# Optimization experiments

Measured on AMD Instinct MI355X. Metric: run time of the kernel, lower is better.

## Reference

```python
import jax, jax.numpy as jnp
import numpy as np

N, DEG, F_IN, H = 50000, 16, 128, 32
E = N * DEG


def _linear_params(key, out_f, in_f):
    kw, kb = jax.random.split(key)
    s = 1.0 / np.sqrt(in_f)
    W = jax.random.uniform(kw, (out_f, in_f), jnp.float32, -s, s)
    b = jax.random.uniform(kb, (out_f,), jnp.float32, -s, s)
    return W, b


def setup_inputs() -> dict:
    key = jax.random.key(0)
    ks = jax.random.split(key, 12)
    X = jax.random.normal(ks[0], (N, F_IN), jnp.float32)
    # DEG distinct nonzero offsets shared by all rows -> unique (src,dst) pairs,
    # so the COO tensor is already coalesced (no duplicate indices).
    offsets = jax.random.permutation(ks[1], jnp.arange(1, N))[:DEG]
    src = jnp.repeat(jnp.arange(N, dtype=jnp.int32), DEG)
    dst = ((src.reshape(N, DEG) + offsets[None, :].astype(jnp.int32)) % N).reshape(-1)
    D = jax.ops.segment_sum(jnp.ones((E,), jnp.float32), src, num_segments=N)
    wn1p, bn1p = _linear_params(ks[2], H, F_IN)      # convN1.pass_map
    wn1s, bn1s = _linear_params(ks[3], H, F_IN)      # convN1.self_map
    we1p, be1p = _linear_params(ks[4], H, 2 * H)     # convE1.pass_map
    we1s, be1s = _linear_params(ks[5], H, F_IN)      # convE1.self_map
    wn2p, bn2p = _linear_params(ks[6], H, H)         # convN2.pass_map
    wn2s, bn2s = _linear_params(ks[7], H, H)         # convN2.self_map
    we2p, be2p = _linear_params(ks[8], H, 2 * H)     # convE2.pass_map
    we2s, be2s = _linear_params(ks[9], H, H)         # convE2.self_map
    wc, bc = _linear_params(ks[10], 1, H)            # classifier
    return dict(X=X, src=src, dst=dst, D=D,
                wn1p=wn1p, bn1p=bn1p, wn1s=wn1s, bn1s=bn1s,
                we1p=we1p, be1p=be1p, we1s=we1s, be1s=be1s,
                wn2p=wn2p, bn2p=bn2p, wn2s=wn2s, bn2s=bn2s,
                we2p=we2p, be2p=be2p, we2s=we2s, be2s=be2s,
                wc=wc, bc=bc)


def reference(X, src, dst, D,
              wn1p, bn1p, wn1s, bn1s,
              we1p, be1p, we1s, be1s,
              wn2p, bn2p, wn2s, bn2s,
              we2p, be2p, we2s, be2s,
              wc, bc):
    n = X.shape[0]

    def node_conv(vals, Xn, wp, bp, ws, bs):
        # torch.sparse.sum(A, dim=1): sum edge values per source row
        Asum = jax.ops.segment_sum(vals, src, num_segments=n)
        return jax.nn.relu((Asum / D[:, None]) @ wp.T + bp + Xn @ ws.T + bs)

    def edge_conv(vals, Xn, wp, bp, ws, bs):
        X1, X2 = Xn[src], Xn[dst]
        Ef = jnp.concatenate([(X1 - X2) * 0.5, (X1 + X2) * 0.5], axis=-1)
        return jax.nn.relu(Ef @ wp.T + bp + vals @ ws.T + bs)

    # add_graph: edge features = |X[src] - X[dst]|
    vals0 = jnp.abs(X[src] - X[dst])            # (E, F_IN)
    X0 = jnp.zeros_like(X)                       # forward zeros node features
    Xn1 = node_conv(vals0, X0, wn1p, bn1p, wn1s, bn1s)   # (N, 32)
    vals1 = edge_conv(vals0, Xn1, we1p, be1p, we1s, be1s)  # (E, 32)
    Xn2 = node_conv(vals1, Xn1, wn2p, bn2p, wn2s, bn2s)  # (N, 32)
    vals2 = edge_conv(vals1, Xn2, we2p, be2p, we2s, be2s)  # (E, 32)
    SX = jax.nn.sigmoid(vals2 @ wc.T + bc)[:, 0]          # (E,)
    return SX
```

## Files before the change

### kernel.cpp

```cpp
#include <hip/hip_runtime.h>

#define DEG 16
#define F_IN 128
#define H 32

typedef __attribute__((ext_vector_type(8))) _Float16 f16x8;
typedef __attribute__((ext_vector_type(4))) float f32x4;
typedef __attribute__((ext_vector_type(4))) int i32x4;

union HS  { _Float16 f; unsigned short s; };
union HF4 { _Float16 h[4]; uint2 u; };

__device__ __forceinline__ float relu_f(float x) { return fmaxf(x, 0.0f); }

__device__ __forceinline__ f16x8 habs8(f16x8 a) {
    union { f16x8 h; i32x4 i; } u; u.h = a;
#pragma unroll
    for (int k = 0; k < 4; ++k) u.i[k] &= 0x7FFF7FFF;
    return u.h;
}

__global__ __launch_bounds__(256) void k_pre(
    const float* __restrict__ X, _Float16* __restrict__ Xh, long n8,
    const float* __restrict__ we1s, const float* __restrict__ we1p,
    const float* __restrict__ be1p, const float* __restrict__ be1s,
    const float* __restrict__ we2p, const float* __restrict__ we2s,
    const float* __restrict__ be2p, const float* __restrict__ be2s,
    const float* __restrict__ wn1p, const float* __restrict__ bn1p,
    const float* __restrict__ bn1s,
    const float* __restrict__ wn2p, const float* __restrict__ bn2p,
    const float* __restrict__ wn2s, const float* __restrict__ bn2s,
    _Float16* __restrict__ Wcat1, _Float16* __restrict__ Wcat2,
    _Float16* __restrict__ Wn1ph,
    _Float16* __restrict__ Wn2ph, _Float16* __restrict__ Wn2sh,
    float* __restrict__ bias1, float* __restrict__ bias2,
    float* __restrict__ biasn1, float* __restrict__ biasn2)
{
    if (blockIdx.x >= 32) {
        const long t = (long)(blockIdx.x - 32) * 256 + threadIdx.x;
        if (t >= n8) return;
        const float4* p = (const float4*)X + t * 2;
        const float4 a = p[0], b = p[1];
        f16x8 h;
        h[0] = (_Float16)a.x; h[1] = (_Float16)a.y; h[2] = (_Float16)a.z; h[3] = (_Float16)a.w;
        h[4] = (_Float16)b.x; h[5] = (_Float16)b.y; h[6] = (_Float16)b.z; h[7] = (_Float16)b.w;
        *(f16x8*)(Xh + t * 8) = h;
        return;
    }
    const int t0 = blockIdx.x * 256 + threadIdx.x;
    const int stride = 32 * 256;
    for (int idx = t0; idx < 32 * 192; idx += stride) {
        const int n = idx / 192, k = idx - n * 192;
        float w;
        if (k < 128)       w = we1s[n * 128 + k];
        else if (k < 160)  w = 0.5f * we1p[n * 64 + (k - 128)];
        else               w = 0.5f * we1p[n * 64 + 32 + (k - 160)];
        Wcat1[idx] = (_Float16)w;
    }
    for (int idx = t0; idx < 32 * 96; idx += stride) {
        const int n = idx / 96, k = idx - n * 96;
        float w;
        if (k < 32)       w = 0.5f * we2p[n * 64 + k];
        else if (k < 64)  w = 0.5f * we2p[n * 64 + 32 + (k - 32)];
        else              w = we2s[n * 32 + (k - 64)];
        Wcat2[idx] = (_Float16)w;
    }
    for (int idx = t0; idx < 32 * 128; idx += stride)
        Wn1ph[idx] = (_Float16)wn1p[idx];
    for (int idx = t0; idx < 32 * 32; idx += stride) {
        Wn2ph[idx] = (_Float16)wn2p[idx];
        Wn2sh[idx] = (_Float16)wn2s[idx];
    }
    if (t0 < H) {
        bias1[t0]  = be1p[t0] + be1s[t0];
        bias2[t0]  = be2p[t0] + be2s[t0];
        biasn1[t0] = bn1p[t0] + bn1s[t0];
        biasn2[t0] = bn2p[t0] + bn2s[t0];
    }
}

__global__ __launch_bounds__(256, 3) void k_p1(
    const _Float16* __restrict__ Xh, const int* __restrict__ dst,
    const float* __restrict__ D,
    const _Float16* __restrict__ Wcat1, const _Float16* __restrict__ Wn1ph,
    const float* __restrict__ biasn1,
    _Float16* __restrict__ t1h, _Float16* __restrict__ Xn1h, int N)
{
    __shared__ float red[4][8][64];
    const int tid = threadIdx.x;
    const int lane = tid & 63;
    const int w = tid >> 6;
    const int m = lane & 15, g = lane >> 4;
    const int i0 = blockIdx.x * 16;
    const int srow = (i0 + m < N) ? (i0 + m) : (N - 1);

    const i32x4 dj = ((const i32x4*)(dst + (size_t)srow * DEG))[w];

    f16x8 sv[4];
#pragma unroll
    for (int kb = 0; kb < 4; ++kb)
        sv[kb] = *(const f16x8*)(Xh + (size_t)srow * F_IN + kb * 32 + g * 8);
    f16x8 Bs[4][2], Bn[4][2];
#pragma unroll
    for (int kb = 0; kb < 4; ++kb)
#pragma unroll
        for (int t = 0; t < 2; ++t) {
            Bs[kb][t] = *(const f16x8*)(Wcat1 + (t * 16 + m) * 192 + kb * 32 + g * 8);
            Bn[kb][t] = *(const f16x8*)(Wn1ph + (t * 16 + m) * 128 + kb * 32 + g * 8);
        }

    f16x8 tvc[4], tvn[4];
#pragma unroll
    for (int kb = 0; kb < 4; ++kb)
        tvc[kb] = *(const f16x8*)(Xh + (size_t)dj[0] * F_IN + kb * 32 + g * 8);

    f32x4 cn0 = {0.f,0.f,0.f,0.f}, cn1 = {0.f,0.f,0.f,0.f};
#pragma unroll
    for (int jj = 0; jj < 4; ++jj) {
        if (jj < 3) {
            const int dn = dj[jj + 1];
#pragma unroll
            for (int kb = 0; kb < 4; ++kb)
                tvn[kb] = *(const f16x8*)(Xh + (size_t)dn * F_IN + kb * 32 + g * 8);
        }
        f32x4 cs0 = {0.f,0.f,0.f,0.f}, cs1 = {0.f,0.f,0.f,0.f};
#pragma unroll
        for (int kb = 0; kb < 4; ++kb) {
            const f16x8 a = habs8(sv[kb] - tvc[kb]);
            cs0 = __builtin_amdgcn_mfma_f32_16x16x32_f16(a, Bs[kb][0], cs0, 0, 0, 0);
            cs1 = __builtin_amdgcn_mfma_f32_16x16x32_f16(a, Bs[kb][1], cs1, 0, 0, 0);
            cn0 = __builtin_amdgcn_mfma_f32_16x16x32_f16(a, Bn[kb][0], cn0, 0, 0, 0);
            cn1 = __builtin_amdgcn_mfma_f32_16x16x32_f16(a, Bn[kb][1], cn1, 0, 0, 0);
        }
        const size_t tb = ((size_t)blockIdx.x * 16 + w * 4 + jj) * 512;
        HF4 a4;
#pragma unroll
        for (int r = 0; r < 4; ++r) a4.h[r] = (_Float16)cs0[r];
        *(uint2*)(t1h + tb + lane * 4) = a4.u;
#pragma unroll
        for (int r = 0; r < 4; ++r) a4.h[r] = (_Float16)cs1[r];
        *(uint2*)(t1h + tb + 256 + lane * 4) = a4.u;
#pragma unroll
        for (int kb = 0; kb < 4; ++kb) tvc[kb] = tvn[kb];
    }
#pragma unroll
    for (int r = 0; r < 4; ++r) {
        red[w][r][lane]     = cn0[r];
        red[w][4 + r][lane] = cn1[r];
    }
    __syncthreads();
    if (w == 0) {
        const float bn0 = biasn1[m], bn1v = biasn1[16 + m];
#pragma unroll
        for (int r = 0; r < 4; ++r) {
            const int node = i0 + g * 4 + r;
            if (node < N) {
                const float invD = 1.0f / D[node];
                const float a0 = red[0][r][lane] + red[1][r][lane]
                               + red[2][r][lane] + red[3][r][lane];
                const float a1 = red[0][4+r][lane] + red[1][4+r][lane]
                               + red[2][4+r][lane] + red[3][4+r][lane];
                Xn1h[(size_t)node * H + m]      = (_Float16)relu_f(a0 * invD + bn0);
                Xn1h[(size_t)node * H + 16 + m] = (_Float16)relu_f(a1 * invD + bn1v);
            }
        }
    }
}

__global__ __launch_bounds__(256, 4) void k_p2(
    const int* __restrict__ dst, const _Float16* __restrict__ Xn1h,
    const _Float16* __restrict__ Wcat1, const float* __restrict__ bias1,
    const _Float16* __restrict__ Wn2ph, const _Float16* __restrict__ Wn2sh,
    const float* __restrict__ biasn2, const float* __restrict__ D,
    _Float16* t1v1,
    _Float16* __restrict__ Xn2h, int N)
{
    __shared__ unsigned short RP[4][16 * 40];
    __shared__ float red[4][8][64];
    const int tid = threadIdx.x;
    const int lane = tid & 63;
    const int w = tid >> 6;
    const int m = lane & 15, g = lane >> 4;
    const int i0 = blockIdx.x * 16;
    const int srow = (i0 + m < N) ? (i0 + m) : (N - 1);

    const i32x4 dj = ((const i32x4*)(dst + (size_t)srow * DEG))[w];
    const f16x8 x1 = *(const f16x8*)(Xn1h + (size_t)srow * H + g * 8);
    f16x8 Bf[2][2];
#pragma unroll
    for (int kb = 0; kb < 2; ++kb)
#pragma unroll
        for (int t = 0; t < 2; ++t)
            Bf[kb][t] = *(const f16x8*)(Wcat1 + (t * 16 + m) * 192 + (4 + kb) * 32 + g * 8);

    f16x8 x2c, x2n;
    uint2 u0c, u1c, u0n, u1n;
    {
        const int d0 = dj[0];
        x2c = *(const f16x8*)(Xn1h + (size_t)d0 * H + g * 8);
        const size_t tb = ((size_t)blockIdx.x * 16 + w * 4) * 512;
        u0c = *(const uint2*)(t1v1 + tb + lane * 4);
        u1c = *(const uint2*)(t1v1 + tb + 256 + lane * 4);
    }
    const float b0 = bias1[m], b1v = bias1[16 + m];
    f32x4 sB0 = {0.f,0.f,0.f,0.f}, sB1 = {0.f,0.f,0.f,0.f};
    const int rr = lane >> 2, qq = lane & 3;
    unsigned short* RPw = RP[w];
#pragma unroll
    for (int jj = 0; jj < 4; ++jj) {
        if (jj < 3) {
            const int dn = dj[jj + 1];
            x2n = *(const f16x8*)(Xn1h + (size_t)dn * H + g * 8);
            const size_t tbn = ((size_t)blockIdx.x * 16 + w * 4 + jj + 1) * 512;
            u0n = *(const uint2*)(t1v1 + tbn + lane * 4);
            u1n = *(const uint2*)(t1v1 + tbn + 256 + lane * 4);
        }
        f32x4 c0, c1;
        { HF4 a; a.u = u0c;
#pragma unroll
          for (int r = 0; r < 4; ++r) c0[r] = (float)a.h[r];
          a.u = u1c;
#pragma unroll
          for (int r = 0; r < 4; ++r) c1[r] = (float)a.h[r]; }
        const f16x8 ad = x1 - x2c;
        const f16x8 aS = x1 + x2c;
        c0 = __builtin_amdgcn_mfma_f32_16x16x32_f16(ad, Bf[0][0], c0, 0, 0, 0);
        c1 = __builtin_amdgcn_mfma_f32_16x16x32_f16(ad, Bf[0][1], c1, 0, 0, 0);
        c0 = __builtin_amdgcn_mfma_f32_16x16x32_f16(aS, Bf[1][0], c0, 0, 0, 0);
        c1 = __builtin_amdgcn_mfma_f32_16x16x32_f16(aS, Bf[1][1], c1, 0, 0, 0);
#pragma unroll
        for (int r = 0; r < 4; ++r) {
            const float v0 = relu_f(c0[r] + b0);
            const float v1 = relu_f(c1[r] + b1v);
            HS h0, h1; h0.f = (_Float16)v0; h1.f = (_Float16)v1;
            RPw[(g * 4 + r) * 40 + m]      = h0.s;
            RPw[(g * 4 + r) * 40 + 16 + m] = h1.s;
            sB0[r] += v0; sB1[r] += v1;
        }
        const size_t tb = ((size_t)blockIdx.x * 16 + w * 4 + jj) * 512;
        const i32x4 v = *(const i32x4*)(RPw + rr * 40 + qq * 8);
        *(i32x4*)(t1v1 + tb + rr * 32 + qq * 8) = v;
        x2c = x2n; u0c = u0n; u1c = u1n;
    }
#pragma unroll
    for (int r = 0; r < 4; ++r) {
        red[w][r][lane]     = sB0[r];
        red[w][4 + r][lane] = sB1[r];
    }
    __syncthreads();
    if (w == 0) {
        _Float16* RPh = (_Float16*)RP[0];
#pragma unroll
        for (int r = 0; r < 4; ++r) {
            const int node = i0 + g * 4 + r;
            const float invD = 1.0f / D[(node < N) ? node : (N - 1)];
            const float a0 = red[0][r][lane] + red[1][r][lane]
                           + red[2][r][lane] + red[3][r][lane];
            const float a1 = red[0][4+r][lane] + red[1][4+r][lane]
                           + red[2][4+r][lane] + red[3][4+r][lane];
            RPh[(g * 4 + r) * 40 + m]      = (_Float16)(a0 * invD);
            RPh[(g * 4 + r) * 40 + 16 + m] = (_Float16)(a1 * invD);
        }
        const f16x8 aF = *(const f16x8*)(RPh + m * 40 + g * 8);
        f16x8 Bp[2], Bs2[2];
#pragma unroll
        for (int t = 0; t < 2; ++t) {
            Bp[t]  = *(const f16x8*)(Wn2ph + (t * 16 + m) * H + g * 8);
            Bs2[t] = *(const f16x8*)(Wn2sh + (t * 16 + m) * H + g * 8);
        }
        f32x4 c0 = {0.f,0.f,0.f,0.f}, c1 = {0.f,0.f,0.f,0.f};
        c0 = __builtin_amdgcn_mfma_f32_16x16x32_f16(aF, Bp[0], c0, 0, 0, 0);
        c1 = __builtin_amdgcn_mfma_f32_16x16x32_f16(aF, Bp[1], c1, 0, 0, 0);
        c0 = __builtin_amdgcn_mfma_f32_16x16x32_f16(x1, Bs2[0], c0, 0, 0, 0);
        c1 = __builtin_amdgcn_mfma_f32_16x16x32_f16(x1, Bs2[1], c1, 0, 0, 0);
        const float bp0 = biasn2[m], bp1 = biasn2[16 + m];
#pragma unroll
        for (int r = 0; r < 4; ++r) {
            const int node = i0 + g * 4 + r;
            if (node < N) {
                Xn2h[(size_t)node * H + m]      = (_Float16)relu_f(c0[r] + bp0);
                Xn2h[(size_t)node * H + 16 + m] = (_Float16)relu_f(c1[r] + bp1);
            }
        }
    }
}

__global__ __launch_bounds__(256, 4) void k_p3(
    const _Float16* __restrict__ Xn2h, const int* __restrict__ dst,
    const _Float16* __restrict__ vals1,
    const _Float16* __restrict__ Wcat2, const float* __restrict__ bias2,
    const float* __restrict__ wc, const float* __restrict__ bc,
    float* __restrict__ out, int N)
{
    __shared__ float outS[16 * 16];
    const int tid = threadIdx.x;
    const int lane = tid & 63;
    const int w = tid >> 6;
    const int m = lane & 15, g = lane >> 4;
    const int i0 = blockIdx.x * 16;
    const int srow = (i0 + m < N) ? (i0 + m) : (N - 1);

    const i32x4 dj = ((const i32x4*)(dst + (size_t)srow * DEG))[w];
    const f16x8 x1 = *(const f16x8*)(Xn2h + (size_t)srow * H + g * 8);
    f16x8 Bf[3][2];
#pragma unroll
    for (int kb = 0; kb < 3; ++kb)
#pragma unroll
        for (int t = 0; t < 2; ++t)
            Bf[kb][t] = *(const f16x8*)(Wcat2 + (t * 16 + m) * 96 + kb * 32 + g * 8);

    f16x8 x2b[2], avb[2];
#pragma unroll
    for (int s = 0; s < 2; ++s) {
        const int dn = dj[s];
        x2b[s] = *(const f16x8*)(Xn2h + (size_t)dn * H + g * 8);
        avb[s] = *(const f16x8*)(vals1 + ((size_t)blockIdx.x * 16 + w * 4 + s) * 512 + m * 32 + g * 8);
    }
    const float b0 = bias2[m], b1v = bias2[16 + m];
    const float w0 = wc[m], w1 = wc[16 + m];
#pragma unroll
    for (int jj = 0; jj < 4; ++jj) {
        const int s = jj & 1;
        const f16x8 x2 = x2b[s];
        const f16x8 av = avb[s];
        if (jj < 2) {
            const int dn = dj[jj + 2];
            x2b[s] = *(const f16x8*)(Xn2h + (size_t)dn * H + g * 8);
            avb[s] = *(const f16x8*)(vals1 + ((size_t)blockIdx.x * 16 + w * 4 + jj + 2) * 512 + m * 32 + g * 8);
        }
        const f16x8 ad = x1 - x2;
        const f16x8 aS = x1 + x2;
        f32x4 c0 = {0.f,0.f,0.f,0.f}, c1 = {0.f,0.f,0.f,0.f};
        c0 = __builtin_amdgcn_mfma_f32_16x16x32_f16(ad, Bf[0][0], c0, 0, 0, 0);
        c1 = __builtin_amdgcn_mfma_f32_16x16x32_f16(ad, Bf[0][1], c1, 0, 0, 0);
        c0 = __builtin_amdgcn_mfma_f32_16x16x32_f16(aS, Bf[1][0], c0, 0, 0, 0);
        c1 = __builtin_amdgcn_mfma_f32_16x16x32_f16(aS, Bf[1][1], c1, 0, 0, 0);
        c0 = __builtin_amdgcn_mfma_f32_16x16x32_f16(av, Bf[2][0], c0, 0, 0, 0);
        c1 = __builtin_amdgcn_mfma_f32_16x16x32_f16(av, Bf[2][1], c1, 0, 0, 0);

        float sr[4];
#pragma unroll
        for (int r = 0; r < 4; ++r)
            sr[r] = relu_f(c0[r] + b0) * w0 + relu_f(c1[r] + b1v) * w1;
#pragma unroll
        for (int mask = 1; mask < 16; mask <<= 1) {
#pragma unroll
            for (int r = 0; r < 4; ++r)
                sr[r] += __shfl_xor(sr[r], mask);
        }
        if (m == 0) {
#pragma unroll
            for (int r = 0; r < 4; ++r)
                outS[(g * 4 + r) * 16 + (w * 4 + jj)] = sr[r];
        }
    }
    __syncthreads();
    {
        const float bcv = bc[0];
        const float v = outS[tid];
        const float o = 1.0f / (1.0f + __expf(-(v + bcv)));
        if (i0 + 16 <= N || (i0 + (tid >> 4)) < N)
            out[(size_t)i0 * DEG + tid] = o;
    }
}

extern "C" void kernel_launch(void* const* d_in, const int* in_sizes, int n_in,
                              void* d_out, int out_size, void* d_ws, size_t ws_size,
                              hipStream_t stream)
{
    const float* X    = (const float*)d_in[0];
    const int*   dst  = (const int*)  d_in[2];
    const float* D    = (const float*)d_in[3];
    const float* wn1p = (const float*)d_in[4];
    const float* bn1p = (const float*)d_in[5];
    const float* bn1s = (const float*)d_in[7];
    const float* we1p = (const float*)d_in[8];
    const float* be1p = (const float*)d_in[9];
    const float* we1s = (const float*)d_in[10];
    const float* be1s = (const float*)d_in[11];
    const float* wn2p = (const float*)d_in[12];
    const float* bn2p = (const float*)d_in[13];
    const float* wn2s = (const float*)d_in[14];
    const float* bn2s = (const float*)d_in[15];
    const float* we2p = (const float*)d_in[16];
    const float* be2p = (const float*)d_in[17];
    const float* we2s = (const float*)d_in[18];
    const float* be2s = (const float*)d_in[19];
    const float* wc   = (const float*)d_in[20];
    const float* bc   = (const float*)d_in[21];

    const int N = in_sizes[3];
    const int nbW = (N + 15) / 16;
    const size_t Epad = (size_t)nbW * 16 * DEG;

    char* w = (char*)d_ws;
    _Float16* t1v1  = (_Float16*)w;  w += Epad * H * 2;
    _Float16* Xh    = (_Float16*)w;  w += (size_t)N * F_IN * 2;
    _Float16* Xn1h  = (_Float16*)w;  w += (size_t)N * H * 2;
    _Float16* Xn2h  = (_Float16*)w;  w += (size_t)N * H * 2;
    _Float16* Wcat1 = (_Float16*)w;  w += 32 * 192 * 2;
    _Float16* Wcat2 = (_Float16*)w;  w += 32 * 96 * 2;
    _Float16* Wn1ph = (_Float16*)w;  w += 32 * 128 * 2;
    _Float16* Wn2ph = (_Float16*)w;  w += 32 * 32 * 2;
    _Float16* Wn2sh = (_Float16*)w;  w += 32 * 32 * 2;
    float* bias1  = (float*)w;       w += H * 4;
    float* bias2  = (float*)w;       w += H * 4;
    float* biasn1 = (float*)w;       w += H * 4;
    float* biasn2 = (float*)w;       w += H * 4;
    float* outp = (float*)d_out;

    const long n8 = (long)N * F_IN / 8;
    const int nbX = (int)((n8 + 255) / 256);

    k_pre<<<nbX + 32, 256, 0, stream>>>(X, Xh, n8,
                                        we1s, we1p, be1p, be1s, we2p, we2s, be2p, be2s,
                                        wn1p, bn1p, bn1s, wn2p, bn2p, wn2s, bn2s,
                                        Wcat1, Wcat2, Wn1ph, Wn2ph, Wn2sh,
                                        bias1, bias2, biasn1, biasn2);
    k_p1<<<nbW, 256, 0, stream>>>(Xh, dst, D, Wcat1, Wn1ph, biasn1, t1v1, Xn1h, N);
    k_p2<<<nbW, 256, 0, stream>>>(dst, Xn1h, Wcat1, bias1, Wn2ph, Wn2sh,
                                  biasn2, D, t1v1, Xn2h, N);
    k_p3<<<nbW, 256, 0, stream>>>(Xn2h, dst, t1v1, Wcat2, bias2, wc, bc, outp, N);
}
```

Measured before the change: 210.3 us.

## Run k_p1 with one wave per 16 nodes and add nontemporal streaming accesses

```diff
diff --git a/kernel.cpp b/kernel.cpp
--- a/kernel.cpp
+++ b/kernel.cpp
@@ -7,9 +7,11 @@
 typedef __attribute__((ext_vector_type(8))) _Float16 f16x8;
 typedef __attribute__((ext_vector_type(4))) float f32x4;
 typedef __attribute__((ext_vector_type(4))) int i32x4;
+typedef __attribute__((ext_vector_type(4))) float fv4;
+typedef __attribute__((ext_vector_type(2))) unsigned int uv2;
 
 union HS  { _Float16 f; unsigned short s; };
-union HF4 { _Float16 h[4]; uint2 u; };
+union HF4 { _Float16 h[4]; uv2 u; };
 
 __device__ __forceinline__ float relu_f(float x) { return fmaxf(x, 0.0f); }
 
@@ -39,11 +41,12 @@
     if (blockIdx.x >= 32) {
         const long t = (long)(blockIdx.x - 32) * 256 + threadIdx.x;
         if (t >= n8) return;
-        const float4* p = (const float4*)X + t * 2;
-        const float4 a = p[0], b = p[1];
+        const fv4* p = (const fv4*)X + t * 2;
+        const fv4 a = __builtin_nontemporal_load(p);
+        const fv4 b = __builtin_nontemporal_load(p + 1);
         f16x8 h;
-        h[0] = (_Float16)a.x; h[1] = (_Float16)a.y; h[2] = (_Float16)a.z; h[3] = (_Float16)a.w;
-        h[4] = (_Float16)b.x; h[5] = (_Float16)b.y; h[6] = (_Float16)b.z; h[7] = (_Float16)b.w;
+        h[0] = (_Float16)a[0]; h[1] = (_Float16)a[1]; h[2] = (_Float16)a[2]; h[3] = (_Float16)a[3];
+        h[4] = (_Float16)b[0]; h[5] = (_Float16)b[1]; h[6] = (_Float16)b[2]; h[7] = (_Float16)b[3];
         *(f16x8*)(Xh + t * 8) = h;
         return;
     }
@@ -79,23 +82,24 @@
     }
 }
 
-__global__ __launch_bounds__(256, 3) void k_p1(
+__global__ __launch_bounds__(64, 3) void k_p1(
     const _Float16* __restrict__ Xh, const int* __restrict__ dst,
     const float* __restrict__ D,
     const _Float16* __restrict__ Wcat1, const _Float16* __restrict__ Wn1ph,
     const float* __restrict__ biasn1,
     _Float16* __restrict__ t1h, _Float16* __restrict__ Xn1h, int N)
 {
-    __shared__ float red[4][8][64];
-    const int tid = threadIdx.x;
-    const int lane = tid & 63;
-    const int w = tid >> 6;
+    const int lane = threadIdx.x;
     const int m = lane & 15, g = lane >> 4;
     const int i0 = blockIdx.x * 16;
     const int srow = (i0 + m < N) ? (i0 + m) : (N - 1);
 
-    const i32x4 dj = ((const i32x4*)(dst + (size_t)srow * DEG))[w];
-
+    i32x4 dj4[4];
+    {
+        const i32x4* dp = (const i32x4*)(dst + (size_t)srow * DEG);
+#pragma unroll
+        for (int q = 0; q < 4; ++q) dj4[q] = dp[q];
+    }
     f16x8 sv[4];
 #pragma unroll
     for (int kb = 0; kb < 4; ++kb)
@@ -112,13 +116,13 @@
     f16x8 tvc[4], tvn[4];
 #pragma unroll
     for (int kb = 0; kb < 4; ++kb)
-        tvc[kb] = *(const f16x8*)(Xh + (size_t)dj[0] * F_IN + kb * 32 + g * 8);
+        tvc[kb] = *(const f16x8*)(Xh + (size_t)dj4[0][0] * F_IN + kb * 32 + g * 8);
 
     f32x4 cn0 = {0.f,0.f,0.f,0.f}, cn1 = {0.f,0.f,0.f,0.f};
 #pragma unroll
-    for (int jj = 0; jj < 4; ++jj) {
-        if (jj < 3) {
-            const int dn = dj[jj + 1];
+    for (int j = 0; j < 16; ++j) {
+        if (j < 15) {
+            const int dn = dj4[(j + 1) >> 2][(j + 1) & 3];
 #pragma unroll
             for (int kb = 0; kb < 4; ++kb)
                 tvn[kb] = *(const f16x8*)(Xh + (size_t)dn * F_IN + kb * 32 + g * 8);
@@ -132,37 +136,25 @@
             cn0 = __builtin_amdgcn_mfma_f32_16x16x32_f16(a, Bn[kb][0], cn0, 0, 0, 0);
             cn1 = __builtin_amdgcn_mfma_f32_16x16x32_f16(a, Bn[kb][1], cn1, 0, 0, 0);
         }
-        const size_t tb = ((size_t)blockIdx.x * 16 + w * 4 + jj) * 512;
-        HF4 a4;
-#pragma unroll
-        for (int r = 0; r < 4; ++r) a4.h[r] = (_Float16)cs0[r];
-        *(uint2*)(t1h + tb + lane * 4) = a4.u;
-#pragma unroll
-        for (int r = 0; r < 4; ++r) a4.h[r] = (_Float16)cs1[r];
-        *(uint2*)(t1h + tb + 256 + lane * 4) = a4.u;
+        const size_t tb = ((size_t)blockIdx.x * 16 + j) * 512;
+        HF4 a;
+#pragma unroll
+        for (int r = 0; r < 4; ++r) a.h[r] = (_Float16)cs0[r];
+        __builtin_nontemporal_store(a.u, (uv2*)(t1h + tb + lane * 4));
+#pragma unroll
+        for (int r = 0; r < 4; ++r) a.h[r] = (_Float16)cs1[r];
+        __builtin_nontemporal_store(a.u, (uv2*)(t1h + tb + 256 + lane * 4));
 #pragma unroll
         for (int kb = 0; kb < 4; ++kb) tvc[kb] = tvn[kb];
     }
+    const float bn0 = biasn1[m], bn1v = biasn1[16 + m];
 #pragma unroll
     for (int r = 0; r < 4; ++r) {
-        red[w][r][lane]     = cn0[r];
-        red[w][4 + r][lane] = cn1[r];
-    }
-    __syncthreads();
-    if (w == 0) {
-        const float bn0 = biasn1[m], bn1v = biasn1[16 + m];
-#pragma unroll
-        for (int r = 0; r < 4; ++r) {
-            const int node = i0 + g * 4 + r;
-            if (node < N) {
-                const float invD = 1.0f / D[node];
-                const float a0 = red[0][r][lane] + red[1][r][lane]
-                               + red[2][r][lane] + red[3][r][lane];
-                const float a1 = red[0][4+r][lane] + red[1][4+r][lane]
-                               + red[2][4+r][lane] + red[3][4+r][lane];
-                Xn1h[(size_t)node * H + m]      = (_Float16)relu_f(a0 * invD + bn0);
-                Xn1h[(size_t)node * H + 16 + m] = (_Float16)relu_f(a1 * invD + bn1v);
-            }
+        const int node = i0 + g * 4 + r;
+        if (node < N) {
+            const float invD = 1.0f / D[node];
+            Xn1h[(size_t)node * H + m]      = (_Float16)relu_f(cn0[r] * invD + bn0);
+            Xn1h[(size_t)node * H + 16 + m] = (_Float16)relu_f(cn1[r] * invD + bn1v);
         }
     }
 }
@@ -194,13 +186,13 @@
             Bf[kb][t] = *(const f16x8*)(Wcat1 + (t * 16 + m) * 192 + (4 + kb) * 32 + g * 8);
 
     f16x8 x2c, x2n;
-    uint2 u0c, u1c, u0n, u1n;
+    uv2 u0c, u1c, u0n, u1n;
     {
         const int d0 = dj[0];
         x2c = *(const f16x8*)(Xn1h + (size_t)d0 * H + g * 8);
         const size_t tb = ((size_t)blockIdx.x * 16 + w * 4) * 512;
-        u0c = *(const uint2*)(t1v1 + tb + lane * 4);
-        u1c = *(const uint2*)(t1v1 + tb + 256 + lane * 4);
+        u0c = __builtin_nontemporal_load((const uv2*)(t1v1 + tb + lane * 4));
+        u1c = __builtin_nontemporal_load((const uv2*)(t1v1 + tb + 256 + lane * 4));
     }
     const float b0 = bias1[m], b1v = bias1[16 + m];
     f32x4 sB0 = {0.f,0.f,0.f,0.f}, sB1 = {0.f,0.f,0.f,0.f};
@@ -212,8 +204,8 @@
             const int dn = dj[jj + 1];
             x2n = *(const f16x8*)(Xn1h + (size_t)dn * H + g * 8);
             const size_t tbn = ((size_t)blockIdx.x * 16 + w * 4 + jj + 1) * 512;
-            u0n = *(const uint2*)(t1v1 + tbn + lane * 4);
-            u1n = *(const uint2*)(t1v1 + tbn + 256 + lane * 4);
+            u0n = __builtin_nontemporal_load((const uv2*)(t1v1 + tbn + lane * 4));
+            u1n = __builtin_nontemporal_load((const uv2*)(t1v1 + tbn + 256 + lane * 4));
         }
         f32x4 c0, c1;
         { HF4 a; a.u = u0c;
@@ -417,7 +409,7 @@
                                         wn1p, bn1p, bn1s, wn2p, bn2p, wn2s, bn2s,
                                         Wcat1, Wcat2, Wn1ph, Wn2ph, Wn2sh,
                                         bias1, bias2, biasn1, biasn2);
-    k_p1<<<nbW, 256, 0, stream>>>(Xh, dst, D, Wcat1, Wn1ph, biasn1, t1v1, Xn1h, N);
+    k_p1<<<nbW, 64, 0, stream>>>(Xh, dst, D, Wcat1, Wn1ph, biasn1, t1v1, Xn1h, N);
     k_p2<<<nbW, 256, 0, stream>>>(dst, Xn1h, Wcat1, bias1, Wn2ph, Wn2sh,
                                   biasn2, D, t1v1, Xn2h, N);
     k_p3<<<nbW, 256, 0, stream>>>(Xn2h, dst, t1v1, Wcat2, bias2, wc, bc, outp, N);
```

Measured after the change: 196.1 us, median of 2. -6.7%, faster.
